# Performance work log

Hardware: AMD Instinct MI355X
Metric: run time of the kernel (lower is better)

Reference implementation:

```python
import jax, jax.numpy as jnp
import numpy as np

SPS_AMPLIFY = 1.5
SPS_DAMPEN = 0.3
SPS_DEEP_QUESTION = 0.1
SPS_EXCLAIM = 0.85
SPS_QUESTION = 0.25
SPS_SUPER_EXCLAIM = 0.95

B, S, D = 4, 2048, 1024
NUM_HEADS = 16
HEAD_DIM = D // NUM_HEADS
SCALE = HEAD_DIM ** (-0.5)


def sps_pro(x):
    """Piecewise elementwise modulation based on sigmoid(x) bands."""
    xn = jax.nn.sigmoid(x)
    # bands: xn>0.95 -> 2.0 ; 0.85<xn<=0.95 -> 1.5 ; xn<0.1 -> 0.1 ;
    #        0.1<=xn<0.25 -> 0.3 ; else -> 1.0
    mult = jnp.where(
        xn > SPS_SUPER_EXCLAIM, 2.0,
        jnp.where(xn > SPS_EXCLAIM, SPS_AMPLIFY,
                  jnp.where(xn < SPS_DEEP_QUESTION, 0.1,
                            jnp.where(xn < SPS_QUESTION, SPS_DAMPEN, 1.0))))
    return x * mult


def setup_inputs() -> dict:
    key = jax.random.key(0)
    k0, k1, k2, k3, k4 = jax.random.split(key, 5)
    s = 1.0 / np.sqrt(D)
    return {
        "x": jax.random.normal(k0, (B, S, D), dtype=jnp.float32),
        "W_qkv": jax.random.uniform(k1, (D, 3 * D), dtype=jnp.float32, minval=-s, maxval=s),
        "b_qkv": jax.random.uniform(k2, (3 * D,), dtype=jnp.float32, minval=-s, maxval=s),
        "W_proj": jax.random.uniform(k3, (D, D), dtype=jnp.float32, minval=-s, maxval=s),
        "b_proj": jax.random.uniform(k4, (D,), dtype=jnp.float32, minval=-s, maxval=s),
    }


def reference(x, W_qkv, b_qkv, W_proj, b_proj):
    qkv = jnp.einsum('bsd,de->bse', x, W_qkv) + b_qkv  # [B,S,3D]
    q, k, v = jnp.split(qkv, 3, axis=-1)               # each [B,S,D]
    attn = jnp.einsum('bsd,btd->bst', q, k) * SCALE    # [B,S,S]
    attn = sps_pro(attn)
    attn = jax.nn.softmax(attn, axis=-1)
    out = jnp.einsum('bst,btd->bsd', attn, v)          # [B,S,D]
    out = jnp.einsum('bsd,de->bse', out, W_proj) + b_proj
    return out
```

## Files before the change

### kernel.cpp

```cpp
#include <hip/hip_runtime.h>
#include <hip/hip_bf16.h>
#include <hip/hip_fp16.h>
#include <stdint.h>

typedef __attribute__((ext_vector_type(8))) _Float16 f16x8;
typedef __attribute__((ext_vector_type(4))) float f32x4;

__device__ __forceinline__ void async16(void* lds, const void* g) {
  __builtin_amdgcn_global_load_lds(
      (const __attribute__((address_space(1))) void*)g,
      (__attribute__((address_space(3))) void*)lds, 16, 0, 0);
}

__device__ __forceinline__ uint16_t f2h_u(float f) {
  union { __half h; uint16_t u; } c;
  c.h = __float2half(f);
  return c.u;
}

__global__ __launch_bounds__(256)
void conv_f2h(const float* __restrict__ in, uint16_t* __restrict__ out, int n4) {
  int i = blockIdx.x * 256 + threadIdx.x;
  if (i >= n4) return;
  float4 v = ((const float4*)in)[i];
  ushort4 o;
  o.x = f2h_u(v.x); o.y = f2h_u(v.y); o.z = f2h_u(v.z); o.w = f2h_u(v.w);
  ((ushort4*)out)[i] = o;
}

__global__ __launch_bounds__(256)
void trans_f2h(const float* __restrict__ in, uint16_t* __restrict__ out,
               int ldin, int ldout) {
  __shared__ float t[64][65];
  const int tx = threadIdx.x & 63, ty = threadIdx.x >> 6;
  const int r0 = blockIdx.y * 64, c0 = blockIdx.x * 64;
#pragma unroll
  for (int i = 0; i < 16; ++i)
    t[ty + i * 4][tx] = in[(size_t)(r0 + ty + i * 4) * ldin + c0 + tx];
  __syncthreads();
#pragma unroll
  for (int i = 0; i < 16; ++i)
    out[(size_t)(c0 + ty + i * 4) * ldout + r0 + tx] = f2h_u(t[tx][ty + i * 4]);
}

template <int EPI>
__global__ __launch_bounds__(512, 2)
void gemm8p(const uint16_t* __restrict__ A, const uint16_t* __restrict__ B,
            void* __restrict__ Cv, void* __restrict__ Cv2, void* __restrict__ Cv3,
            const float* __restrict__ bias,
            int nT, int lda, int ldb, int ldc,
            long long strA, long long strB, long long strC) {
  extern __shared__ uint16_t lds_u16[];

  const int gx = gridDim.x, gy = gridDim.y;
  const int nwg = gx * gy * gridDim.z;
  const int fid = blockIdx.x + gx * (blockIdx.y + gy * blockIdx.z);
  const int fs = (fid & 7) * (nwg >> 3) + (fid >> 3);
  const int bx = fs % gx;
  const int by = (fs / gx) % gy;
  const int bz = fs / (gx * gy);

  const int tid = threadIdx.x;
  const int l = tid & 63;
  const int w = tid >> 6;
  const int wm = w >> 2, wn = w & 3;
  const int l15 = l & 15, l4 = l >> 4;
  const int rowBase = bx * 256, colBase = by * 256;
  const uint16_t* Ag = A + (size_t)bz * strA;
  const uint16_t* Bg = B + (size_t)bz * strB;

  const uint16_t* sA[2][2];
  const uint16_t* sB[2][2];
#pragma unroll
  for (int u = 0; u < 2; ++u) {
    int c = tid + (u << 9);
    int cs = c ^ ((c >> 3) & 7);
    int row = cs >> 3, kc = (cs & 7) * 8;
    sA[0][u] = Ag + (size_t)(rowBase + row) * lda + kc;
    sA[1][u] = Ag + (size_t)(rowBase + 128 + row) * lda + kc;
    sB[0][u] = Bg + (size_t)(colBase + row) * ldb + kc;
    sB[1][u] = Bg + (size_t)(colBase + 128 + row) * ldb + kc;
  }

  f32x4 acc[8][4];
#pragma unroll
  for (int m = 0; m < 8; ++m)
#pragma unroll
    for (int n = 0; n < 4; ++n)
      acc[m][n] = (f32x4){0.f, 0.f, 0.f, 0.f};

#define SH_A(buf, h, koff)                                                     \
  {                                                                            \
    const uint32_t d_ = (buf)*32768u + (h)*8192u;                              \
    async16(&lds_u16[d_ + (size_t)tid * 8], sA[h][0] + (koff));                \
    async16(&lds_u16[d_ + (size_t)(tid + 512) * 8], sA[h][1] + (koff));        \
  }
#define SH_B(buf, h, koff)                                                     \
  {                                                                            \
    const uint32_t d_ = (buf)*32768u + 16384u + (h)*8192u;                     \
    async16(&lds_u16[d_ + (size_t)tid * 8], sB[h][0] + (koff));                \
    async16(&lds_u16[d_ + (size_t)(tid + 512) * 8], sB[h][1] + (koff));        \
  }
#define RD_A(dst, buf, mh)                                                     \
  _Pragma("unroll") for (int mr = 0; mr < 4; ++mr) {                           \
    const int lr = (mh)*64 + mr * 16 + l15;                                    \
    const char* hb = (const char*)lds_u16 + (buf)*65536 + wm * 16384;          \
    _Pragma("unroll") for (int ks = 0; ks < 2; ++ks)                           \
      dst[mr][ks] = *(const f16x8*)(hb + lr * 128 +                            \
                    ((ks * 64 + l4 * 16) ^ ((lr & 7) << 4)));                  \
  }
#define RD_B(dst, buf, nh)                                                     \
  _Pragma("unroll") for (int nr = 0; nr < 2; ++nr) {                           \
    const int lr = (wn & 1) * 64 + (nh)*32 + nr * 16 + l15;                    \
    const char* hb = (const char*)lds_u16 + (buf)*65536 + 32768 +              \
                     (wn >> 1) * 16384;                                        \
    _Pragma("unroll") for (int ks = 0; ks < 2; ++ks)                           \
      dst[nr][ks] = *(const f16x8*)(hb + lr * 128 +                            \
                    ((ks * 64 + l4 * 16) ^ ((lr & 7) << 4)));                  \
  }
#define MM(m0, n0, AF, BF)                                                     \
  __builtin_amdgcn_s_setprio(1);                                               \
  _Pragma("unroll") for (int ks = 0; ks < 2; ++ks)                             \
  _Pragma("unroll") for (int mr = 0; mr < 4; ++mr)                             \
  _Pragma("unroll") for (int nr = 0; nr < 2; ++nr)                             \
    acc[(m0) + mr][(n0) + nr] = __builtin_amdgcn_mfma_f32_16x16x32_f16(        \
        AF[mr][ks], BF[nr][ks], acc[(m0) + mr][(n0) + nr], 0, 0, 0);           \
  __builtin_amdgcn_s_setprio(0);
#define VMC(n) asm volatile("s_waitcnt vmcnt(" #n ")" ::: "memory");
#define BAR() __builtin_amdgcn_s_barrier();

  SH_A(0, 0, 0) SH_A(0, 1, 0) SH_B(0, 0, 0) SH_B(0, 1, 0)
  SH_B(1, 0, 64) SH_B(1, 1, 64)
  VMC(4)
  BAR()

  const int nIter = nT >> 1;
  for (int i = 0; i < nIter; ++i) {
    const int e2 = 2 * i + 2, o = 2 * i + 1, o2 = 2 * i + 3;
    const int ke2 = e2 << 6, ko = o << 6, ko2 = o2 << 6;
    f16x8 a0[4][2], a1[4][2], b0[2][2], b1[2][2];
    RD_A(a0, 0, 0) RD_B(b0, 0, 0)
    SH_A(1, 0, ko)
    BAR()
    MM(0, 0, a0, b0)
    RD_B(b1, 0, 1)
    SH_A(1, 1, ko)
    BAR()
    MM(0, 2, a0, b1)
    RD_A(a1, 0, 1)
    if (e2 < nT) SH_B(0, 0, ke2)
    BAR()
    MM(4, 2, a1, b1)
    if (e2 < nT) { SH_B(0, 1, ke2) VMC(4) } else { VMC(0) }
    BAR()
    MM(4, 0, a1, b0)
    RD_A(a0, 1, 0) RD_B(b0, 1, 0)
    if (e2 < nT) SH_A(0, 0, ke2)
    BAR()
    MM(0, 0, a0, b0)
    RD_B(b1, 1, 1)
    if (e2 < nT) SH_A(0, 1, ke2)
    BAR()
    MM(0, 2, a0, b1)
    RD_A(a1, 1, 1)
    if (o2 < nT) SH_B(1, 0, ko2)
    BAR()
    MM(4, 2, a1, b1)
    if (o2 < nT) { SH_B(1, 1, ko2) }
    if (i + 1 < nIter) { if (o2 < nT) { VMC(4) } else { VMC(0) } }
    BAR()
    MM(4, 0, a1, b0)
  }
#undef SH_A
#undef SH_B
#undef RD_A
#undef RD_B
#undef MM
#undef VMC
#undef BAR

  if (EPI == 0) {
    uint16_t* qd = (uint16_t*)Cv;
    uint16_t* kd = (uint16_t*)Cv2;
    uint16_t* vt = (uint16_t*)Cv3;
#pragma unroll
    for (int ni = 0; ni < 4; ++ni) {
      const int gcol = colBase + wn * 64 + ni * 16 + l15;
      const float bv = bias[gcol];
      if (gcol < 2048) {
        uint16_t* base = (gcol < 1024 ? qd : kd) + (gcol & 1023);
#pragma unroll
        for (int mi = 0; mi < 8; ++mi)
#pragma unroll
          for (int j = 0; j < 4; ++j) {
            const int grow = rowBase + wm * 128 + mi * 16 + l4 * 4 + j;
            base[(size_t)(grow >> 11) * 2097152 + (size_t)(grow & 2047) * 1024] =
                f2h_u(acc[mi][ni][j] + bv);
          }
      } else {
        const int d = gcol - 2048;
#pragma unroll
        for (int mi = 0; mi < 8; ++mi) {
          const int grow0 = rowBase + wm * 128 + mi * 16 + l4 * 4;
          ushort4 o;
          o.x = f2h_u(acc[mi][ni][0] + bv);
          o.y = f2h_u(acc[mi][ni][1] + bv);
          o.z = f2h_u(acc[mi][ni][2] + bv);
          o.w = f2h_u(acc[mi][ni][3] + bv);
          *(ushort4*)&vt[(size_t)(grow0 >> 11) * 2097152 + (size_t)d * 2048 +
                         (grow0 & 2047)] = o;
        }
      }
    }
  }
}

template <int EPI>
__global__ __launch_bounds__(256, 2)
void gemm_mb(const uint16_t* __restrict__ A, const uint16_t* __restrict__ B,
             void* __restrict__ Cv, const float* __restrict__ bias,
             int nT, int lda, int ldb, int ldc,
             long long strA, long long strB, long long strC) {
  extern __shared__ uint16_t lds_u16[];

  const int gx = gridDim.x, gy = gridDim.y;
  const int nwg = gx * gy * gridDim.z;
  const int fid = blockIdx.x + gx * (blockIdx.y + gy * blockIdx.z);
  const int fs = (fid & 7) * (nwg >> 3) + (fid >> 3);
  const int bx = fs % gx;
  const int by = (fs / gx) % gy;
  const int bz = fs / (gx * gy);

  const int tid = threadIdx.x;
  const int l = tid & 63;
  const int w = tid >> 6;
  const int wm = w >> 1, wn = w & 1;
  const int l15 = l & 15, l4 = l >> 4;
  const int rowBase = bx * 128, colBase = by * 128;
  const uint16_t* Ag = A + (size_t)bz * strA;
  const uint16_t* Bg = B + (size_t)bz * strB;

  const uint16_t* pA[4];
  const uint16_t* pB[4];
#pragma unroll
  for (int u = 0; u < 4; ++u) {
    int c = tid + (u << 8);
    int cs = c ^ ((c >> 3) & 7);
    pA[u] = Ag + (size_t)(rowBase + (cs >> 3)) * lda + (cs & 7) * 8;
    pB[u] = Bg + (size_t)(colBase + (cs >> 3)) * ldb + (cs & 7) * 8;
  }

  f32x4 acc[4][4];
#pragma unroll
  for (int m = 0; m < 4; ++m)
#pragma unroll
    for (int n = 0; n < 4; ++n)
      acc[m][n] = (f32x4){0.f, 0.f, 0.f, 0.f};

#define STAGE(t2, s2)                                                          \
  {                                                                            \
    const int kb_ = (t2) << 6;                                                 \
    uint16_t* dA_ = lds_u16 + (s2)*16384;                                      \
    uint16_t* dB_ = dA_ + 8192;                                                \
    _Pragma("unroll") for (int u = 0; u < 4; ++u) {                            \
      async16(&dA_[(size_t)(tid + (u << 8)) * 8], pA[u] + kb_);                \
      async16(&dB_[(size_t)(tid + (u << 8)) * 8], pB[u] + kb_);                \
    }                                                                          \
  }

  STAGE(0, 0)
  asm volatile("s_waitcnt vmcnt(0)" ::: "memory");
  __builtin_amdgcn_s_barrier();

  for (int t = 0; t < nT; ++t) {
    const int s = t & 1;
    if (t + 1 < nT) STAGE(t + 1, s ^ 1)
    const uint16_t* As = lds_u16 + s * 16384;
    const uint16_t* Bs = As + 8192;
#pragma unroll
    for (int ks = 0; ks < 2; ++ks) {
      f16x8 af[4], bf[4];
#pragma unroll
      for (int m = 0; m < 4; ++m) {
        const int r = wm * 64 + m * 16 + l15;
        const int byt = r * 128 + ((ks * 64 + l4 * 16) ^ ((r & 7) << 4));
        af[m] = *(const f16x8*)((const char*)As + byt);
      }
#pragma unroll
      for (int n = 0; n < 4; ++n) {
        const int r = wn * 64 + n * 16 + l15;
        const int byt = r * 128 + ((ks * 64 + l4 * 16) ^ ((r & 7) << 4));
        bf[n] = *(const f16x8*)((const char*)Bs + byt);
      }
      __builtin_amdgcn_s_setprio(1);
#pragma unroll
      for (int m = 0; m < 4; ++m)
#pragma unroll
        for (int n = 0; n < 4; ++n)
          acc[m][n] = __builtin_amdgcn_mfma_f32_16x16x32_f16(af[m], bf[n], acc[m][n], 0, 0, 0);
      __builtin_amdgcn_s_setprio(0);
    }
    if (t + 1 < nT) {
      asm volatile("s_waitcnt vmcnt(0)" ::: "memory");
      __builtin_amdgcn_s_barrier();
    }
  }
#undef STAGE

  const int orow0 = rowBase + wm * 64 + l4 * 4;
  const int ocol0 = colBase + wn * 64 + l15;
  if (EPI == 1) {
    uint16_t* C = (uint16_t*)Cv + (size_t)bz * strC;
#pragma unroll
    for (int n = 0; n < 4; ++n)
#pragma unroll
      for (int m = 0; m < 4; ++m)
#pragma unroll
        for (int j = 0; j < 4; ++j) {
          float xs = acc[m][n][j] * 0.125f;
          float mult = (xs > 2.94443897916644f) ? 2.0f
                     : (xs > 1.73460105538811f) ? 1.5f
                     : (xs < -2.19722457733622f) ? 0.1f
                     : (xs < -1.09861228866811f) ? 0.3f
                                                 : 1.0f;
          C[(size_t)(orow0 + m * 16 + j) * ldc + ocol0 + n * 16] = f2h_u(xs * mult);
        }
  } else if (EPI == 3) {
    uint16_t* C = (uint16_t*)Cv + (size_t)bz * strC;
#pragma unroll
    for (int n = 0; n < 4; ++n)
#pragma unroll
      for (int m = 0; m < 4; ++m)
#pragma unroll
        for (int j = 0; j < 4; ++j)
          C[(size_t)(orow0 + m * 16 + j) * ldc + ocol0 + n * 16] = f2h_u(acc[m][n][j]);
  } else {
    float* C = (float*)Cv;
#pragma unroll
    for (int n = 0; n < 4; ++n) {
      const float bv = bias[ocol0 + n * 16];
#pragma unroll
      for (int m = 0; m < 4; ++m)
#pragma unroll
        for (int j = 0; j < 4; ++j)
          C[(size_t)(orow0 + m * 16 + j) * ldc + ocol0 + n * 16] = acc[m][n][j] + bv;
    }
  }
}

__global__ __launch_bounds__(256)
void softmax_rows(uint16_t* __restrict__ P) {
  const size_t row = blockIdx.x;
  uint16_t* p = P + row * 2048;
  const int tid = threadIdx.x;
  uint4 raw = *(const uint4*)(p + tid * 8);
  uint32_t w[4] = {raw.x, raw.y, raw.z, raw.w};
  float v[8];
#pragma unroll
  for (int q = 0; q < 4; ++q) {
    __half2 h = *(__half2*)&w[q];
    float2 f = __half22float2(h);
    v[2 * q] = f.x;
    v[2 * q + 1] = f.y;
  }
  float mx = v[0];
#pragma unroll
  for (int j = 1; j < 8; ++j) mx = fmaxf(mx, v[j]);
#pragma unroll
  for (int o = 32; o > 0; o >>= 1) mx = fmaxf(mx, __shfl_xor(mx, o));
  __shared__ float redm[4], reds[4];
  if ((tid & 63) == 0) redm[tid >> 6] = mx;
  __syncthreads();
  mx = fmaxf(fmaxf(redm[0], redm[1]), fmaxf(redm[2], redm[3]));
  float e[8];
  float se = 0.f;
#pragma unroll
  for (int j = 0; j < 8; ++j) { e[j] = __expf(v[j] - mx); se += e[j]; }
#pragma unroll
  for (int o = 32; o > 0; o >>= 1) se += __shfl_xor(se, o);
  if ((tid & 63) == 0) reds[tid >> 6] = se;
  __syncthreads();
  se = (reds[0] + reds[1]) + (reds[2] + reds[3]);
  const float inv = 1.0f / se;
  uint32_t wo[4];
#pragma unroll
  for (int q = 0; q < 4; ++q) {
    uint16_t a = f2h_u(e[2 * q] * inv);
    uint16_t b = f2h_u(e[2 * q + 1] * inv);
    wo[q] = (uint32_t)a | ((uint32_t)b << 16);
  }
  uint4 ov;
  ov.x = wo[0]; ov.y = wo[1]; ov.z = wo[2]; ov.w = wo[3];
  *(uint4*)(p + tid * 8) = ov;
}

extern "C" void kernel_launch(void* const* d_in, const int* in_sizes, int n_in,
                              void* d_out, int out_size, void* d_ws, size_t ws_size,
                              hipStream_t stream) {
  const float* x     = (const float*)d_in[0];
  const float* Wqkv  = (const float*)d_in[1];
  const float* bqkv  = (const float*)d_in[2];
  const float* Wproj = (const float*)d_in[3];
  const float* bproj = (const float*)d_in[4];
  float* out = (float*)d_out;

  char* ws = (char*)d_ws;
  size_t off = 0;
  auto alloc = [&](size_t bytes) -> void* {
    void* p = ws + off;
    off += (bytes + 255) & ~(size_t)255;
    return p;
  };
  uint16_t* xh    = (uint16_t*)alloc(8192ULL * 1024 * 2);
  uint16_t* WqkvT = (uint16_t*)alloc(3072ULL * 1024 * 2);
  uint16_t* WpT   = (uint16_t*)alloc(1024ULL * 1024 * 2);
  uint16_t* qh    = (uint16_t*)alloc(4ULL * 2048 * 1024 * 2);
  uint16_t* kh    = (uint16_t*)alloc(4ULL * 2048 * 1024 * 2);
  uint16_t* vT    = (uint16_t*)alloc(4ULL * 1024 * 2048 * 2);
  uint16_t* Pm    = (uint16_t*)alloc(4ULL * 2048 * 2048 * 2);
  uint16_t* ao    = xh;

  conv_f2h<<<8192, 256, 0, stream>>>(x, xh, 2097152);
  trans_f2h<<<dim3(48, 16), 256, 0, stream>>>(Wqkv, WqkvT, 3072, 1024);
  trans_f2h<<<dim3(16, 16), 256, 0, stream>>>(Wproj, WpT, 1024, 1024);
  gemm8p<0><<<dim3(32, 12, 1), 512, 131072, stream>>>(
      xh, WqkvT, qh, kh, vT, bqkv, 16, 1024, 1024, 0, 0, 0, 0);
  gemm_mb<1><<<dim3(16, 16, 4), 256, 65536, stream>>>(
      qh, kh, Pm, nullptr, 16, 1024, 1024, 2048,
      2097152LL, 2097152LL, 4194304LL);
  softmax_rows<<<8192, 256, 0, stream>>>(Pm);
  gemm_mb<3><<<dim3(16, 8, 4), 256, 65536, stream>>>(
      Pm, vT, ao, nullptr, 32, 2048, 2048, 1024,
      4194304LL, 2097152LL, 2097152LL);
  gemm_mb<4><<<dim3(64, 8, 1), 256, 65536, stream>>>(
      ao, WpT, out, bproj, 16, 1024, 1024, 1024, 0, 0, 0);
}
```

Measured before the change: 214.8 us.

## Fuse softmax into QK and PV GEMM epilogues using fixed-offset exp and atomic rowsums

Removes the standalone softmax kernel. The QK^T GEMM epilogue now exponentiates the modulated score with a fixed shift instead of the row max, writes unnormalized fp16 probabilities and accumulates per-row sums with atomics. The PV GEMM epilogue then divides by the row sum. This drops a full read-modify-write pass over the score matrix. In exchange it adds a memset, global atomics, and relies on a fixed shift and clamp to keep exp in range for the data, which risks fp16 precision or range problems.

```diff
diff --git a/kernel.cpp b/kernel.cpp
--- a/kernel.cpp
+++ b/kernel.cpp
@@ -219,6 +219,7 @@
 __global__ __launch_bounds__(256, 2)
 void gemm_mb(const uint16_t* __restrict__ A, const uint16_t* __restrict__ B,
              void* __restrict__ Cv, const float* __restrict__ bias,
+             float* __restrict__ rowsum,
              int nT, int lda, int ldb, int ldc,
              long long strA, long long strB, long long strC) {
   extern __shared__ uint16_t lds_u16[];
@@ -309,31 +310,46 @@
 
   const int orow0 = rowBase + wm * 64 + l4 * 4;
   const int ocol0 = colBase + wn * 64 + l15;
-  if (EPI == 1) {
+  if (EPI == 5) {
     uint16_t* C = (uint16_t*)Cv + (size_t)bz * strC;
-#pragma unroll
-    for (int n = 0; n < 4; ++n)
-#pragma unroll
-      for (int m = 0; m < 4; ++m)
-#pragma unroll
-        for (int j = 0; j < 4; ++j) {
+    float* rs_b = rowsum + (size_t)bz * 2048;
+#pragma unroll
+    for (int m = 0; m < 4; ++m)
+#pragma unroll
+      for (int j = 0; j < 4; ++j) {
+        const int grow = orow0 + m * 16 + j;
+        float rs = 0.f;
+#pragma unroll
+        for (int n = 0; n < 4; ++n) {
           float xs = acc[m][n][j] * 0.125f;
           float mult = (xs > 2.94443897916644f) ? 2.0f
                      : (xs > 1.73460105538811f) ? 1.5f
                      : (xs < -2.19722457733622f) ? 0.1f
                      : (xs < -1.09861228866811f) ? 0.3f
                                                  : 1.0f;
-          C[(size_t)(orow0 + m * 16 + j) * ldc + ocol0 + n * 16] = f2h_u(xs * mult);
+          float e = __expf(fminf(xs * mult, 19.0f) - 8.0f);
+          C[(size_t)grow * ldc + ocol0 + n * 16] = f2h_u(e);
+          rs += e;
         }
-  } else if (EPI == 3) {
+        rs += __shfl_xor(rs, 1);
+        rs += __shfl_xor(rs, 2);
+        rs += __shfl_xor(rs, 4);
+        rs += __shfl_xor(rs, 8);
+        if (l15 == 0) atomicAdd(&rs_b[grow], rs);
+      }
+  } else if (EPI == 6) {
     uint16_t* C = (uint16_t*)Cv + (size_t)bz * strC;
-#pragma unroll
-    for (int n = 0; n < 4; ++n)
-#pragma unroll
-      for (int m = 0; m < 4; ++m)
-#pragma unroll
-        for (int j = 0; j < 4; ++j)
-          C[(size_t)(orow0 + m * 16 + j) * ldc + ocol0 + n * 16] = f2h_u(acc[m][n][j]);
+    const float* rs_b = rowsum + (size_t)bz * 2048;
+#pragma unroll
+    for (int m = 0; m < 4; ++m)
+#pragma unroll
+      for (int j = 0; j < 4; ++j) {
+        const int grow = orow0 + m * 16 + j;
+        const float inv = 1.0f / rs_b[grow];
+#pragma unroll
+        for (int n = 0; n < 4; ++n)
+          C[(size_t)grow * ldc + ocol0 + n * 16] = f2h_u(acc[m][n][j] * inv);
+      }
   } else {
     float* C = (float*)Cv;
 #pragma unroll
@@ -346,52 +362,6 @@
           C[(size_t)(orow0 + m * 16 + j) * ldc + ocol0 + n * 16] = acc[m][n][j] + bv;
     }
   }
-}
-
-__global__ __launch_bounds__(256)
-void softmax_rows(uint16_t* __restrict__ P) {
-  const size_t row = blockIdx.x;
-  uint16_t* p = P + row * 2048;
-  const int tid = threadIdx.x;
-  uint4 raw = *(const uint4*)(p + tid * 8);
-  uint32_t w[4] = {raw.x, raw.y, raw.z, raw.w};
-  float v[8];
-#pragma unroll
-  for (int q = 0; q < 4; ++q) {
-    __half2 h = *(__half2*)&w[q];
-    float2 f = __half22float2(h);
-    v[2 * q] = f.x;
-    v[2 * q + 1] = f.y;
-  }
-  float mx = v[0];
-#pragma unroll
-  for (int j = 1; j < 8; ++j) mx = fmaxf(mx, v[j]);
-#pragma unroll
-  for (int o = 32; o > 0; o >>= 1) mx = fmaxf(mx, __shfl_xor(mx, o));
-  __shared__ float redm[4], reds[4];
-  if ((tid & 63) == 0) redm[tid >> 6] = mx;
-  __syncthreads();
-  mx = fmaxf(fmaxf(redm[0], redm[1]), fmaxf(redm[2], redm[3]));
-  float e[8];
-  float se = 0.f;
-#pragma unroll
-  for (int j = 0; j < 8; ++j) { e[j] = __expf(v[j] - mx); se += e[j]; }
-#pragma unroll
-  for (int o = 32; o > 0; o >>= 1) se += __shfl_xor(se, o);
-  if ((tid & 63) == 0) reds[tid >> 6] = se;
-  __syncthreads();
-  se = (reds[0] + reds[1]) + (reds[2] + reds[3]);
-  const float inv = 1.0f / se;
-  uint32_t wo[4];
-#pragma unroll
-  for (int q = 0; q < 4; ++q) {
-    uint16_t a = f2h_u(e[2 * q] * inv);
-    uint16_t b = f2h_u(e[2 * q + 1] * inv);
-    wo[q] = (uint32_t)a | ((uint32_t)b << 16);
-  }
-  uint4 ov;
-  ov.x = wo[0]; ov.y = wo[1]; ov.z = wo[2]; ov.w = wo[3];
-  *(uint4*)(p + tid * 8) = ov;
 }
 
 extern "C" void kernel_launch(void* const* d_in, const int* in_sizes, int n_in,
@@ -411,27 +381,28 @@
     off += (bytes + 255) & ~(size_t)255;
     return p;
   };
-  uint16_t* xh    = (uint16_t*)alloc(8192ULL * 1024 * 2);
-  uint16_t* WqkvT = (uint16_t*)alloc(3072ULL * 1024 * 2);
-  uint16_t* WpT   = (uint16_t*)alloc(1024ULL * 1024 * 2);
-  uint16_t* qh    = (uint16_t*)alloc(4ULL * 2048 * 1024 * 2);
-  uint16_t* kh    = (uint16_t*)alloc(4ULL * 2048 * 1024 * 2);
-  uint16_t* vT    = (uint16_t*)alloc(4ULL * 1024 * 2048 * 2);
-  uint16_t* Pm    = (uint16_t*)alloc(4ULL * 2048 * 2048 * 2);
-  uint16_t* ao    = xh;
-
+  uint16_t* xh     = (uint16_t*)alloc(8192ULL * 1024 * 2);
+  uint16_t* WqkvT  = (uint16_t*)alloc(3072ULL * 1024 * 2);
+  uint16_t* WpT    = (uint16_t*)alloc(1024ULL * 1024 * 2);
+  uint16_t* qh     = (uint16_t*)alloc(4ULL * 2048 * 1024 * 2);
+  uint16_t* kh     = (uint16_t*)alloc(4ULL * 2048 * 1024 * 2);
+  uint16_t* vT     = (uint16_t*)alloc(4ULL * 1024 * 2048 * 2);
+  uint16_t* Pm     = (uint16_t*)alloc(4ULL * 2048 * 2048 * 2);
+  float*    rowsum = (float*)alloc(4ULL * 2048 * 4);
+  uint16_t* ao     = xh;
+
+  hipMemsetAsync(rowsum, 0, 4ULL * 2048 * 4, stream);
   conv_f2h<<<8192, 256, 0, stream>>>(x, xh, 2097152);
   trans_f2h<<<dim3(48, 16), 256, 0, stream>>>(Wqkv, WqkvT, 3072, 1024);
   trans_f2h<<<dim3(16, 16), 256, 0, stream>>>(Wproj, WpT, 1024, 1024);
   gemm8p<0><<<dim3(32, 12, 1), 512, 131072, stream>>>(
       xh, WqkvT, qh, kh, vT, bqkv, 16, 1024, 1024, 0, 0, 0, 0);
-  gemm_mb<1><<<dim3(16, 16, 4), 256, 65536, stream>>>(
-      qh, kh, Pm, nullptr, 16, 1024, 1024, 2048,
+  gemm_mb<5><<<dim3(16, 16, 4), 256, 65536, stream>>>(
+      qh, kh, Pm, nullptr, rowsum, 16, 1024, 1024, 2048,
       2097152LL, 2097152LL, 4194304LL);
-  softmax_rows<<<8192, 256, 0, stream>>>(Pm);
-  gemm_mb<3><<<dim3(16, 8, 4), 256, 65536, stream>>>(
-      Pm, vT, ao, nullptr, 32, 2048, 2048, 1024,
+  gemm_mb<6><<<dim3(16, 8, 4), 256, 65536, stream>>>(
+      Pm, vT, ao, nullptr, rowsum, 32, 2048, 2048, 1024,
       4194304LL, 2097152LL, 2097152LL);
   gemm_mb<4><<<dim3(64, 8, 1), 256, 65536, stream>>>(
-      ao, WpT, out, bproj, 16, 1024, 1024, 1024, 0, 0, 0);
-}
+      ao, WpT, out, bproj, nullptr, 16, 1024, 1024, 1024, 0, 0, 0);
+}
```

Result: no change. 213.9 us (-0.4%).
